# Kernel tuning notes

Measured on AMD Instinct MI355X. Metric: run time of the kernel, lower is better.

## Reference

```python
import jax, jax.numpy as jnp
import numpy as np

N_NODES = 50000
N_EDGES = 800000
HID = 128


def setup_inputs() -> dict:
    key = jax.random.key(0)
    ks = jax.random.split(key, 10)
    s_msg = 1.0 / np.sqrt(2 * HID + 1)
    s_u1 = 1.0 / np.sqrt(2 * HID)
    s_u2 = 1.0 / np.sqrt(HID)
    return {
        "z": jax.random.normal(ks[0], (N_NODES, HID), dtype=jnp.float32),
        "edge_weight": jax.random.uniform(ks[1], (N_EDGES,), dtype=jnp.float32),
        "edge_src": jax.random.randint(ks[2], (N_EDGES,), 0, N_NODES),
        "edge_dst": jax.random.randint(ks[3], (N_EDGES,), 0, N_NODES),
        "Wm": jax.random.normal(ks[4], (2 * HID + 1, HID), dtype=jnp.float32) * s_msg,
        "bm": jax.random.normal(ks[5], (HID,), dtype=jnp.float32) * s_msg,
        "W1": jax.random.normal(ks[6], (2 * HID, HID), dtype=jnp.float32) * s_u1,
        "b1": jax.random.normal(ks[7], (HID,), dtype=jnp.float32) * s_u1,
        "W2": jax.random.normal(ks[8], (HID, HID), dtype=jnp.float32) * s_u2,
        "b2": jax.random.normal(ks[9], (HID,), dtype=jnp.float32) * s_u2,
    }


def reference(z, edge_weight, edge_src, edge_dst, Wm, bm, W1, b1, W2, b2):
    n, H = z.shape
    # message Linear on concat([z[u], z[v], w]) split to avoid materializing [E, 2H+1]
    Wd, Ws, ww = Wm[:H], Wm[H:2 * H], Wm[2 * H]  # [H,H], [H,H], [H]
    msgs = (z[edge_dst] @ Wd + z[edge_src] @ Ws
            + edge_weight[:, None] * ww[None, :] + bm)  # [E, H]
    # max-aggregate messages per destination node; zeros for isolated nodes
    agg = jax.ops.segment_max(msgs, edge_dst, num_segments=n)  # [n, H], -inf if empty
    deg = jax.ops.segment_sum(jnp.ones_like(edge_weight), edge_dst, num_segments=n)
    agg = jnp.where(deg[:, None] > 0, agg, jnp.zeros((), dtype=z.dtype))
    # update MLP on concat([z, agg]) split into two GEMMs
    W1a, W1b = W1[:H], W1[H:]
    hidden = jax.nn.relu(z @ W1a + agg @ W1b + b1)  # [n, H]
    return hidden @ W2 + b2  # [n, H]
```

## Files before the change

kernel.cpp:

```cpp
#include <hip/hip_runtime.h>
#include <hip/hip_bf16.h>

#define HID 128

typedef short bf16x8 __attribute__((ext_vector_type(8)));
typedef float f32x4  __attribute__((ext_vector_type(4)));
typedef unsigned short u16;
typedef unsigned long long u64;

__device__ __forceinline__ u16 f2bf(float f) {
    __hip_bfloat16 h = __float2bfloat16(f);
    return *reinterpret_cast<u16*>(&h);
}
__device__ __forceinline__ float bf2f(u16 x) {
    unsigned u = ((unsigned)x) << 16;
    return __uint_as_float(u);
}
__device__ __forceinline__ u64 pack_rec(int dst, int src, float w) {
    int wq = (int)fmaf(w, 32768.f, 0.5f);
    wq = wq > 32767 ? 32767 : wq;
    return ((u64)(unsigned)dst << 31) | ((unsigned)src << 15) | (unsigned)wq;
}


__global__ __launch_bounds__(256)
void prep_hist(const float* __restrict__ z, const float* __restrict__ Wm,
               const float* __restrict__ W1, const float* __restrict__ W2,
               const int* __restrict__ edst,
               u16* __restrict__ Ab, u16* __restrict__ Wt, int* __restrict__ bhist,
               int N, int Mp, int E, int bz, int bw, int nbk)
{
    __shared__ int lh[256];
    const int b = blockIdx.x;
    const int t = threadIdx.x;
    if (b < bz) {
        const int idx4 = (b * 256 + t) * 4;
        if (idx4 >= Mp * 128) return;
        const int row = idx4 >> 7, col = idx4 & 127;
        ushort4 u;
        if (row < N) {
            const float4 v = *(const float4*)&z[(size_t)row * 128 + col];
            u.x = f2bf(v.x); u.y = f2bf(v.y); u.z = f2bf(v.z); u.w = f2bf(v.w);
        } else { u.x = 0; u.y = 0; u.z = 0; u.w = 0; }
        *(ushort4*)&Ab[(size_t)row * 256 + col] = u;
    } else if (b < bz + bw) {
        const int idx = (b - bz) * 256 + t;
        if (idx >= 81920) return;
        float v;
        if (idx < 32768) {
            const int nn = idx >> 7, k = idx & 127;
            v = (nn < 128) ? Wm[k * 128 + nn] : Wm[(128 + k) * 128 + (nn - 128)];
        } else if (idx < 65536) {
            const int j = idx - 32768, n = j >> 8, k = j & 255;
            v = W1[k * 128 + n];
        } else {
            const int j = idx - 65536, n = j >> 7, k = j & 127;
            v = W2[k * 128 + n];
        }
        Wt[idx] = f2bf(v);
    } else {
        lh[t] = 0;
        __syncthreads();
        const int e0 = (b - bz - bw) * 4096;
        const int eend = min(e0 + 4096, E);
        for (int e = e0 + t; e < eend; e += 256)
            atomicAdd(&lh[edst[e] >> 8], 1);
        __syncthreads();
        if (t < nbk && lh[t] > 0) atomicAdd(&bhist[t], lh[t]);
    }
}

__global__ __launch_bounds__(256)
void scatter_gemmP(const int* __restrict__ esrc, const int* __restrict__ edst,
                   const float* __restrict__ ew,
                   const int* __restrict__ bhist, int* __restrict__ brun,
                   u64* __restrict__ tmp, int E, int nbk, int nsc,
                   const u16* __restrict__ Ab, const u16* __restrict__ Wds_t,
                   u16* __restrict__ Pb, int Mp)
{
    __shared__ int cnt[256];
    __shared__ int rbase[256];
    __shared__ int bbase[256];
    __shared__ u16 As[64 * 136];
    const int t = threadIdx.x;

    if (blockIdx.x < nsc) {
        const int e0 = blockIdx.x * 4096;
        const int eend = min(e0 + 4096, E);

        cnt[t] = 0;
        if (t == 0) {
            int run = 0;
            for (int i = 0; i < nbk; i++) { bbase[i] = run; run += bhist[i]; }
        }
        __syncthreads();

        if (eend - e0 == 4096) {
            int myb[16]; u64 myrec[16];
#pragma unroll
            for (int i = 0; i < 16; i++) {
                const int e = e0 + t + i * 256;
                const int d = edst[e];
                myb[i] = d >> 8;
                myrec[i] = pack_rec(d, esrc[e], ew[e]);
                atomicAdd(&cnt[myb[i]], 1);
            }
            __syncthreads();
            if (t < nbk && cnt[t] > 0) rbase[t] = bbase[t] + atomicAdd(&brun[t], cnt[t]);
            __syncthreads();
            cnt[t] = 0;
            __syncthreads();
#pragma unroll
            for (int i = 0; i < 16; i++) {
                const int r = atomicAdd(&cnt[myb[i]], 1);
                tmp[(size_t)rbase[myb[i]] + r] = myrec[i];
            }
        } else {
            for (int e = e0 + t; e < eend; e += 256)
                atomicAdd(&cnt[edst[e] >> 8], 1);
            __syncthreads();
            if (t < nbk && cnt[t] > 0) rbase[t] = bbase[t] + atomicAdd(&brun[t], cnt[t]);
            __syncthreads();
            cnt[t] = 0;
            __syncthreads();
            for (int e = e0 + t; e < eend; e += 256) {
                const int d = edst[e];
                const int bk = d >> 8;
                const int r = atomicAdd(&cnt[bk], 1);
                tmp[(size_t)rbase[bk] + r] = pack_rec(d, esrc[e], ew[e]);
            }
        }
    } else {
        const int row0 = (blockIdx.x - nsc) * 64;
        const int wv = t >> 6, lane = t & 63;
        const int wy = wv & 1, wx = wv >> 1;
        const int q = lane >> 4, n = lane & 15;

#pragma unroll
        for (int i = 0; i < 4; i++) {
            const int chunk = i * 256 + t;
            const int row = chunk >> 4;
            const int c8 = chunk & 15;
            *(bf16x8*)&As[row * 136 + c8 * 8] =
                *(const bf16x8*)&Ab[(size_t)(row0 + row) * 256 + c8 * 8];
        }
        __syncthreads();

        const u16* pAl = As + (wy * 32 + n) * 136 + q * 8;
        const u16* pB = Wds_t + (size_t)(wx * 128 + n) * 128 + q * 8;

        f32x4 acc[2][8];
#pragma unroll
        for (int i = 0; i < 2; i++)
#pragma unroll
            for (int j = 0; j < 8; j++) acc[i][j] = f32x4{0.f, 0.f, 0.f, 0.f};

#pragma unroll
        for (int kk = 0; kk < 128; kk += 32) {
            bf16x8 a0 = *(const bf16x8*)(pAl + kk);
            bf16x8 a1 = *(const bf16x8*)(pAl + 16 * 136 + kk);
            bf16x8 bfr[8];
#pragma unroll
            for (int ni = 0; ni < 8; ni++)
                bfr[ni] = *(const bf16x8*)(pB + (size_t)ni * 16 * 128 + kk);
#pragma unroll
            for (int ni = 0; ni < 8; ni++) {
                acc[0][ni] = __builtin_amdgcn_mfma_f32_16x16x32_bf16(a0, bfr[ni], acc[0][ni], 0, 0, 0);
                acc[1][ni] = __builtin_amdgcn_mfma_f32_16x16x32_bf16(a1, bfr[ni], acc[1][ni], 0, 0, 0);
            }
        }

#pragma unroll
        for (int mi = 0; mi < 2; mi++) {
#pragma unroll
            for (int ni = 0; ni < 8; ni++) {
                const int rbase2 = row0 + wy * 32 + mi * 16 + q * 4;
                const int c = wx * 128 + ni * 16 + n;
#pragma unroll
                for (int r = 0; r < 4; r++)
                    Pb[(size_t)(rbase2 + r) * 256 + c] = f2bf(acc[mi][ni][r]);
            }
        }
    }
}

__global__ __launch_bounds__(256)
void bucket_sort(const u64* __restrict__ tmp, const int* __restrict__ bhist,
                 int* __restrict__ offsets, unsigned* __restrict__ s_ew,
                 int N, int E, int nbk)
{
    __shared__ int cnt[256];
    __shared__ int cur[256];
    __shared__ int ps[256];
    __shared__ int sh_base[2];
    const int b = blockIdx.x;
    const int t = threadIdx.x;
    const int n0 = b << 8;
    const int nhi = min(256, N - n0);

    if (t == 0) {
        int run = 0;
        for (int i = 0; i < b; i++) run += bhist[i];
        sh_base[0] = run;
        sh_base[1] = run + bhist[b];
    }
    cnt[t] = 0;
    __syncthreads();
    const int base = sh_base[0];
    const int endp = sh_base[1];

    for (int r = base + t; r < endp; r += 256)
        atomicAdd(&cnt[(int)(tmp[r] >> 31) - n0], 1);
    __syncthreads();

    const int v = cnt[t];
    ps[t] = v;
    __syncthreads();
    for (int off = 1; off < 256; off <<= 1) {
        int add = (t >= off) ? ps[t - off] : 0;
        __syncthreads();
        ps[t] += add;
        __syncthreads();
    }
    cur[t] = base + ps[t] - v;
    __syncthreads();

    if (t < nhi) offsets[n0 + t] = cur[t];
    if (t == 0 && n0 + nhi == N) offsets[N] = E;

    for (int r = base + t; r < endp; r += 256) {
        const u64 rec = tmp[r];
        const int local = (int)(rec >> 31) - n0;
        const int pos = atomicAdd(&cur[local], 1);
        s_ew[pos] = (unsigned)(rec & 0x7FFFFFFFu);
    }
}

__global__ __launch_bounds__(256)
void aggregate_kernel(const u16* __restrict__ Pb,
                      const float* __restrict__ bm,
                      const float* __restrict__ ww,
                      const int* __restrict__ offsets,
                      const unsigned* __restrict__ s_ew,
                      u16* __restrict__ Ab, int N, int Mp)
{
    const int t = threadIdx.x;
    const int lane = t & 63;
    const int g = lane >> 4;
    const int c0 = (lane & 15) * 8;
    const int nd = blockIdx.x * 4 + (t >> 6);
    if (nd >= Mp) return;

    u16* dst = &Ab[(size_t)nd * 256 + 128 + c0];

    int start = 0, end = 0;
    if (nd < N) { start = offsets[nd]; end = offsets[nd + 1]; }

    if (end <= start) {
        if (g == 0) {
            bf16x8 zv = {0, 0, 0, 0, 0, 0, 0, 0};
            *(bf16x8*)dst = zv;
        }
        return;
    }

    float wwv[8];
    {
        const float4 wa = *(const float4*)&ww[c0];
        const float4 wb = *(const float4*)&ww[c0 + 4];
        wwv[0] = wa.x; wwv[1] = wa.y; wwv[2] = wa.z; wwv[3] = wa.w;
        wwv[4] = wb.x; wwv[5] = wb.y; wwv[6] = wb.z; wwv[7] = wb.w;
    }

    const float kq = 1.f / 32768.f;
    float m[8];
#pragma unroll
    for (int j = 0; j < 8; j++) m[j] = -INFINITY;

    const int last = end - 1;
    for (int eb = start; eb < end; eb += 8) {
        int ea = eb + g;      if (ea > last) ea = last;
        int ec = eb + 4 + g;  if (ec > last) ec = last;
        const unsigned u0 = s_ew[ea];
        const unsigned u1 = s_ew[ec];
        const bf16x8 p0 = *(const bf16x8*)&Pb[(size_t)(u0 >> 15) * 256 + 128 + c0];
        const bf16x8 p1 = *(const bf16x8*)&Pb[(size_t)(u1 >> 15) * 256 + 128 + c0];
        const float wA = (float)(u0 & 32767u) * kq;
        const float wB = (float)(u1 & 32767u) * kq;
#pragma unroll
        for (int j = 0; j < 8; j++)
            m[j] = fmaxf(m[j], fmaf(wA, wwv[j], bf2f((u16)p0[j])));
#pragma unroll
        for (int j = 0; j < 8; j++)
            m[j] = fmaxf(m[j], fmaf(wB, wwv[j], bf2f((u16)p1[j])));
    }

#pragma unroll
    for (int j = 0; j < 8; j++) {
        m[j] = fmaxf(m[j], __shfl_xor(m[j], 16));
        m[j] = fmaxf(m[j], __shfl_xor(m[j], 32));
    }

    if (g == 0) {
        const bf16x8 zd = *(const bf16x8*)&Pb[(size_t)nd * 256 + c0];
        const float4 ba = *(const float4*)&bm[c0];
        const float4 bb = *(const float4*)&bm[c0 + 4];
        const float bmv[8] = {ba.x, ba.y, ba.z, ba.w, bb.x, bb.y, bb.z, bb.w};
        bf16x8 outv;
#pragma unroll
        for (int j = 0; j < 8; j++)
            outv[j] = (short)f2bf(bf2f((u16)zd[j]) + bmv[j] + m[j]);
        *(bf16x8*)dst = outv;
    }
}

__global__ __launch_bounds__(256)
void gemm_HO(const u16* __restrict__ Ab, const u16* __restrict__ W1t,
             const float* __restrict__ b1, const u16* __restrict__ W2t,
             const float* __restrict__ b2, float* __restrict__ out, int Mstore)
{
    __shared__ u16 smem[64 * 264];

    const int row0 = blockIdx.x * 64;
    const int tid = threadIdx.x;
    const int wv = tid >> 6, lane = tid & 63;
    const int wy = wv & 1, wx = wv >> 1;
    const int q = lane >> 4, n = lane & 15;

#pragma unroll
    for (int i = 0; i < 8; i++) {
        const int chunk = i * 256 + tid;
        const int row = chunk >> 5;
        const int c8 = chunk & 31;
        *(bf16x8*)&smem[row * 264 + c8 * 8] =
            *(const bf16x8*)&Ab[(size_t)(row0 + row) * 256 + c8 * 8];
    }
    __syncthreads();

    f32x4 acc[2][4];

    {
        const u16* pAl = smem + (wy * 32 + n) * 264 + q * 8;
        const u16* pB = W1t + (size_t)(wx * 64 + n) * 256 + q * 8;

#pragma unroll
        for (int i = 0; i < 2; i++)
#pragma unroll
            for (int j = 0; j < 4; j++) acc[i][j] = f32x4{0.f, 0.f, 0.f, 0.f};

#pragma unroll
        for (int kk = 0; kk < 256; kk += 32) {
            bf16x8 b0 = *(const bf16x8*)(pB + kk);
            bf16x8 b1f = *(const bf16x8*)(pB + 16 * 256 + kk);
            bf16x8 b2f = *(const bf16x8*)(pB + 32 * 256 + kk);
            bf16x8 b3f = *(const bf16x8*)(pB + 48 * 256 + kk);
            bf16x8 a0 = *(const bf16x8*)(pAl + kk);
            bf16x8 a1 = *(const bf16x8*)(pAl + 16 * 264 + kk);
            acc[0][0] = __builtin_amdgcn_mfma_f32_16x16x32_bf16(a0, b0,  acc[0][0], 0, 0, 0);
            acc[0][1] = __builtin_amdgcn_mfma_f32_16x16x32_bf16(a0, b1f, acc[0][1], 0, 0, 0);
            acc[0][2] = __builtin_amdgcn_mfma_f32_16x16x32_bf16(a0, b2f, acc[0][2], 0, 0, 0);
            acc[0][3] = __builtin_amdgcn_mfma_f32_16x16x32_bf16(a0, b3f, acc[0][3], 0, 0, 0);
            acc[1][0] = __builtin_amdgcn_mfma_f32_16x16x32_bf16(a1, b0,  acc[1][0], 0, 0, 0);
            acc[1][1] = __builtin_amdgcn_mfma_f32_16x16x32_bf16(a1, b1f, acc[1][1], 0, 0, 0);
            acc[1][2] = __builtin_amdgcn_mfma_f32_16x16x32_bf16(a1, b2f, acc[1][2], 0, 0, 0);
            acc[1][3] = __builtin_amdgcn_mfma_f32_16x16x32_bf16(a1, b3f, acc[1][3], 0, 0, 0);
        }
    }
    __syncthreads();

#pragma unroll
    for (int mi = 0; mi < 2; mi++) {
#pragma unroll
        for (int ni = 0; ni < 4; ni++) {
            const int rl = wy * 32 + mi * 16 + q * 4;
            const int c = wx * 64 + ni * 16 + n;
#pragma unroll
            for (int r = 0; r < 4; r++) {
                float v = acc[mi][ni][r] + b1[c];
                smem[(rl + r) * 136 + c] = f2bf(fmaxf(v, 0.f));
            }
        }
    }
    __syncthreads();

    {
        const u16* pB = W2t + (size_t)(wx * 64 + n) * 128 + q * 8;
        const u16* pHl = smem + (wy * 32 + n) * 136 + q * 8;

#pragma unroll
        for (int i = 0; i < 2; i++)
#pragma unroll
            for (int j = 0; j < 4; j++) acc[i][j] = f32x4{0.f, 0.f, 0.f, 0.f};

#pragma unroll
        for (int kk = 0; kk < 128; kk += 32) {
            bf16x8 b0 = *(const bf16x8*)(pB + kk);
            bf16x8 b1f = *(const bf16x8*)(pB + 16 * 128 + kk);
            bf16x8 b2f = *(const bf16x8*)(pB + 32 * 128 + kk);
            bf16x8 b3f = *(const bf16x8*)(pB + 48 * 128 + kk);
            bf16x8 a0 = *(const bf16x8*)(pHl + kk);
            bf16x8 a1 = *(const bf16x8*)(pHl + 16 * 136 + kk);
            acc[0][0] = __builtin_amdgcn_mfma_f32_16x16x32_bf16(a0, b0,  acc[0][0], 0, 0, 0);
            acc[0][1] = __builtin_amdgcn_mfma_f32_16x16x32_bf16(a0, b1f, acc[0][1], 0, 0, 0);
            acc[0][2] = __builtin_amdgcn_mfma_f32_16x16x32_bf16(a0, b2f, acc[0][2], 0, 0, 0);
            acc[0][3] = __builtin_amdgcn_mfma_f32_16x16x32_bf16(a0, b3f, acc[0][3], 0, 0, 0);
            acc[1][0] = __builtin_amdgcn_mfma_f32_16x16x32_bf16(a1, b0,  acc[1][0], 0, 0, 0);
            acc[1][1] = __builtin_amdgcn_mfma_f32_16x16x32_bf16(a1, b1f, acc[1][1], 0, 0, 0);
            acc[1][2] = __builtin_amdgcn_mfma_f32_16x16x32_bf16(a1, b2f, acc[1][2], 0, 0, 0);
            acc[1][3] = __builtin_amdgcn_mfma_f32_16x16x32_bf16(a1, b3f, acc[1][3], 0, 0, 0);
        }

#pragma unroll
        for (int mi = 0; mi < 2; mi++) {
#pragma unroll
            for (int ni = 0; ni < 4; ni++) {
                const int rbase = row0 + wy * 32 + mi * 16 + q * 4;
                const int c = wx * 64 + ni * 16 + n;
#pragma unroll
                for (int r = 0; r < 4; r++) {
                    const int rr = rbase + r;
                    if (rr >= Mstore) continue;
                    out[(size_t)rr * 128 + c] = acc[mi][ni][r] + b2[c];
                }
            }
        }
    }
}

extern "C" void kernel_launch(void* const* d_in, const int* in_sizes, int n_in,
                              void* d_out, int out_size, void* d_ws, size_t ws_size,
                              hipStream_t stream) {
    const float* z    = (const float*)d_in[0];
    const float* ew   = (const float*)d_in[1];
    const int*   esrc = (const int*)d_in[2];
    const int*   edst = (const int*)d_in[3];
    const float* Wm   = (const float*)d_in[4];
    const float* bm   = (const float*)d_in[5];
    const float* W1   = (const float*)d_in[6];
    const float* b1   = (const float*)d_in[7];
    const float* W2   = (const float*)d_in[8];
    const float* b2   = (const float*)d_in[9];
    float* out = (float*)d_out;

    const int N  = in_sizes[0] / HID;
    const int E  = in_sizes[1];
    const int Mp = ((N + 63) / 64) * 64;
    const int nbk = (N + 255) / 256;

    char* w = (char*)d_ws;
    u16*  Ab      = (u16*)w;      w += (size_t)Mp * 256 * 2;
    u16*  Pb      = (u16*)w;      w += (size_t)Mp * 256 * 2;
    u16*  Wt      = (u16*)w;      w += (size_t)81920 * 2;
    int*  offsets = (int*)w;      w += (size_t)(N + 64) * 4;
    int*  bhist   = (int*)w;      w += 256 * 4;
    int*  brun    = (int*)w;      w += 256 * 4;
    unsigned* s_ew = (unsigned*)w; w += (size_t)E * 4;
    u64*  tmp     = (u64*)w;      w += (size_t)E * 8;

    const int bz = (Mp * 32 + 255) / 256;
    const int bw = (81920 + 255) / 256;
    const int bh = (E + 4095) / 4096;
    const int nsc = (E + 4095) / 4096;

    hipMemsetAsync(bhist, 0, 512 * sizeof(int), stream);
    prep_hist<<<bz + bw + bh, 256, 0, stream>>>(z, Wm, W1, W2, edst, Ab, Wt, bhist,
                                                N, Mp, E, bz, bw, nbk);
    scatter_gemmP<<<nsc + Mp / 64, 256, 0, stream>>>(esrc, edst, ew, bhist, brun,
                                                     tmp, E, nbk, nsc,
                                                     Ab, Wt, Pb, Mp);
    bucket_sort<<<nbk, 256, 0, stream>>>(tmp, bhist, offsets, s_ew, N, E, nbk);
    aggregate_kernel<<<(Mp + 3) / 4, 256, 0, stream>>>(Pb, bm, Wm + 256 * 128,
                                                       offsets, s_ew, Ab, N, Mp);
    gemm_HO<<<Mp / 64, 256, 0, stream>>>(Ab, Wt + 32768, b1, Wt + 65536, b2, out, N);
}
```

Baseline: 210.0 us.

## Fuse max-aggregation into update GEMM kernel, writing aggregates to shared memory

Merges the separate aggregate kernel into the update-MLP GEMM kernel. Each wave aggregates 16 destination nodes and writes results directly into the shared-memory A tile, which avoids a global round trip of the aggregate half of Ab and one kernel launch. The edge loop is also unrolled to process 16 edges per iteration with a tree of max operations. In exchange, parallelism for the gather phase drops to Mp/64 blocks with serial per-node loops inside each wave, which can cause load imbalance and less latency hiding.

```diff
diff --git a/kernel.cpp b/kernel.cpp
--- a/kernel.cpp
+++ b/kernel.cpp
@@ -237,106 +237,111 @@
 }
 
 __global__ __launch_bounds__(256)
-void aggregate_kernel(const u16* __restrict__ Pb,
-                      const float* __restrict__ bm,
-                      const float* __restrict__ ww,
-                      const int* __restrict__ offsets,
-                      const unsigned* __restrict__ s_ew,
-                      u16* __restrict__ Ab, int N, int Mp)
-{
-    const int t = threadIdx.x;
-    const int lane = t & 63;
-    const int g = lane >> 4;
-    const int c0 = (lane & 15) * 8;
-    const int nd = blockIdx.x * 4 + (t >> 6);
-    if (nd >= Mp) return;
-
-    u16* dst = &Ab[(size_t)nd * 256 + 128 + c0];
-
-    int start = 0, end = 0;
-    if (nd < N) { start = offsets[nd]; end = offsets[nd + 1]; }
-
-    if (end <= start) {
-        if (g == 0) {
-            bf16x8 zv = {0, 0, 0, 0, 0, 0, 0, 0};
-            *(bf16x8*)dst = zv;
-        }
-        return;
-    }
-
-    float wwv[8];
-    {
-        const float4 wa = *(const float4*)&ww[c0];
-        const float4 wb = *(const float4*)&ww[c0 + 4];
-        wwv[0] = wa.x; wwv[1] = wa.y; wwv[2] = wa.z; wwv[3] = wa.w;
-        wwv[4] = wb.x; wwv[5] = wb.y; wwv[6] = wb.z; wwv[7] = wb.w;
-    }
-
-    const float kq = 1.f / 32768.f;
-    float m[8];
-#pragma unroll
-    for (int j = 0; j < 8; j++) m[j] = -INFINITY;
-
-    const int last = end - 1;
-    for (int eb = start; eb < end; eb += 8) {
-        int ea = eb + g;      if (ea > last) ea = last;
-        int ec = eb + 4 + g;  if (ec > last) ec = last;
-        const unsigned u0 = s_ew[ea];
-        const unsigned u1 = s_ew[ec];
-        const bf16x8 p0 = *(const bf16x8*)&Pb[(size_t)(u0 >> 15) * 256 + 128 + c0];
-        const bf16x8 p1 = *(const bf16x8*)&Pb[(size_t)(u1 >> 15) * 256 + 128 + c0];
-        const float wA = (float)(u0 & 32767u) * kq;
-        const float wB = (float)(u1 & 32767u) * kq;
-#pragma unroll
-        for (int j = 0; j < 8; j++)
-            m[j] = fmaxf(m[j], fmaf(wA, wwv[j], bf2f((u16)p0[j])));
-#pragma unroll
-        for (int j = 0; j < 8; j++)
-            m[j] = fmaxf(m[j], fmaf(wB, wwv[j], bf2f((u16)p1[j])));
-    }
-
-#pragma unroll
-    for (int j = 0; j < 8; j++) {
-        m[j] = fmaxf(m[j], __shfl_xor(m[j], 16));
-        m[j] = fmaxf(m[j], __shfl_xor(m[j], 32));
-    }
-
-    if (g == 0) {
-        const bf16x8 zd = *(const bf16x8*)&Pb[(size_t)nd * 256 + c0];
-        const float4 ba = *(const float4*)&bm[c0];
-        const float4 bb = *(const float4*)&bm[c0 + 4];
-        const float bmv[8] = {ba.x, ba.y, ba.z, ba.w, bb.x, bb.y, bb.z, bb.w};
-        bf16x8 outv;
-#pragma unroll
-        for (int j = 0; j < 8; j++)
-            outv[j] = (short)f2bf(bf2f((u16)zd[j]) + bmv[j] + m[j]);
-        *(bf16x8*)dst = outv;
-    }
-}
-
-__global__ __launch_bounds__(256)
-void gemm_HO(const u16* __restrict__ Ab, const u16* __restrict__ W1t,
-             const float* __restrict__ b1, const u16* __restrict__ W2t,
-             const float* __restrict__ b2, float* __restrict__ out, int Mstore)
+void gemm_AHO(const u16* __restrict__ Ab, const u16* __restrict__ Pb,
+              const float* __restrict__ bm, const float* __restrict__ ww,
+              const int* __restrict__ offsets, const unsigned* __restrict__ s_ew,
+              const u16* __restrict__ W1t, const float* __restrict__ b1,
+              const u16* __restrict__ W2t, const float* __restrict__ b2,
+              float* __restrict__ out, int N, int Mstore)
 {
     __shared__ u16 smem[64 * 264];
 
     const int row0 = blockIdx.x * 64;
     const int tid = threadIdx.x;
     const int wv = tid >> 6, lane = tid & 63;
+
+#pragma unroll
+    for (int i = 0; i < 4; i++) {
+        const int chunk = i * 256 + tid;
+        const int row = chunk >> 4;
+        const int c8 = chunk & 15;
+        *(bf16x8*)&smem[row * 264 + c8 * 8] =
+            *(const bf16x8*)&Ab[(size_t)(row0 + row) * 256 + c8 * 8];
+    }
+
+    {
+        const int g = lane >> 4;
+        const int c0 = (lane & 15) * 8;
+        const int ndw0 = row0 + wv * 16;
+
+        const int off_l = offsets[min(ndw0 + min(lane, 16), N)];
+
+        float wwv[8];
+        {
+            const float4 wa = *(const float4*)&ww[c0];
+            const float4 wb = *(const float4*)&ww[c0 + 4];
+            wwv[0] = wa.x; wwv[1] = wa.y; wwv[2] = wa.z; wwv[3] = wa.w;
+            wwv[4] = wb.x; wwv[5] = wb.y; wwv[6] = wb.z; wwv[7] = wb.w;
+        }
+        float bmv[8];
+        {
+            const float4 ba = *(const float4*)&bm[c0];
+            const float4 bb = *(const float4*)&bm[c0 + 4];
+            bmv[0] = ba.x; bmv[1] = ba.y; bmv[2] = ba.z; bmv[3] = ba.w;
+            bmv[4] = bb.x; bmv[5] = bb.y; bmv[6] = bb.z; bmv[7] = bb.w;
+        }
+        const float kq = 1.f / 32768.f;
+
+        for (int i = 0; i < 16; i++) {
+            const int nd = ndw0 + i;
+            const int start = __shfl(off_l, i);
+            const int end   = __shfl(off_l, i + 1);
+            bf16x8 outv = {0, 0, 0, 0, 0, 0, 0, 0};
+
+            if (nd < N && end > start) {
+                float m[8];
+#pragma unroll
+                for (int j = 0; j < 8; j++) m[j] = -INFINITY;
+
+                const int last = end - 1;
+                for (int eb = start; eb < end; eb += 16) {
+                    int ea = eb + g;       if (ea > last) ea = last;
+                    int eb1 = eb + 4 + g;  if (eb1 > last) eb1 = last;
+                    int ec = eb + 8 + g;   if (ec > last) ec = last;
+                    int ed = eb + 12 + g;  if (ed > last) ed = last;
+                    const unsigned u0 = s_ew[ea];
+                    const unsigned u1 = s_ew[eb1];
+                    const unsigned u2 = s_ew[ec];
+                    const unsigned u3 = s_ew[ed];
+                    const bf16x8 p0 = *(const bf16x8*)&Pb[(size_t)(u0 >> 15) * 256 + 128 + c0];
+                    const bf16x8 p1 = *(const bf16x8*)&Pb[(size_t)(u1 >> 15) * 256 + 128 + c0];
+                    const bf16x8 p2 = *(const bf16x8*)&Pb[(size_t)(u2 >> 15) * 256 + 128 + c0];
+                    const bf16x8 p3 = *(const bf16x8*)&Pb[(size_t)(u3 >> 15) * 256 + 128 + c0];
+                    const float wA = (float)(u0 & 32767u) * kq;
+                    const float wB = (float)(u1 & 32767u) * kq;
+                    const float wC = (float)(u2 & 32767u) * kq;
+                    const float wD = (float)(u3 & 32767u) * kq;
+#pragma unroll
+                    for (int j = 0; j < 8; j++) {
+                        const float a = fmaxf(fmaf(wA, wwv[j], bf2f((u16)p0[j])),
+                                              fmaf(wB, wwv[j], bf2f((u16)p1[j])));
+                        const float b = fmaxf(fmaf(wC, wwv[j], bf2f((u16)p2[j])),
+                                              fmaf(wD, wwv[j], bf2f((u16)p3[j])));
+                        m[j] = fmaxf(m[j], fmaxf(a, b));
+                    }
+                }
+
+#pragma unroll
+                for (int j = 0; j < 8; j++) {
+                    m[j] = fmaxf(m[j], __shfl_xor(m[j], 16));
+                    m[j] = fmaxf(m[j], __shfl_xor(m[j], 32));
+                }
+
+                if (g == 0) {
+                    const bf16x8 zd = *(const bf16x8*)&Pb[(size_t)nd * 256 + c0];
+#pragma unroll
+                    for (int j = 0; j < 8; j++)
+                        outv[j] = (short)f2bf(bf2f((u16)zd[j]) + bmv[j] + m[j]);
+                }
+            }
+            if (g == 0)
+                *(bf16x8*)&smem[(nd - row0) * 264 + 128 + c0] = outv;
+        }
+    }
+    __syncthreads();
+
     const int wy = wv & 1, wx = wv >> 1;
     const int q = lane >> 4, n = lane & 15;
-
-#pragma unroll
-    for (int i = 0; i < 8; i++) {
-        const int chunk = i * 256 + tid;
-        const int row = chunk >> 5;
-        const int c8 = chunk & 31;
-        *(bf16x8*)&smem[row * 264 + c8 * 8] =
-            *(const bf16x8*)&Ab[(size_t)(row0 + row) * 256 + c8 * 8];
-    }
-    __syncthreads();
-
     f32x4 acc[2][4];
 
     {
@@ -469,7 +474,7 @@
                                                      tmp, E, nbk, nsc,
                                                      Ab, Wt, Pb, Mp);
     bucket_sort<<<nbk, 256, 0, stream>>>(tmp, bhist, offsets, s_ew, N, E, nbk);
-    aggregate_kernel<<<(Mp + 3) / 4, 256, 0, stream>>>(Pb, bm, Wm + 256 * 128,
-                                                       offsets, s_ew, Ab, N, Mp);
-    gemm_HO<<<Mp / 64, 256, 0, stream>>>(Ab, Wt + 32768, b1, Wt + 65536, b2, out, N);
-}
+    gemm_AHO<<<Mp / 64, 256, 0, stream>>>(Ab, Pb, bm, Wm + 256 * 128,
+                                          offsets, s_ew,
+                                          Wt + 32768, b1, Wt + 65536, b2, out, N, N);
+}
```

New measurement: 215.7 us. +2.7%, slower.
